# Optimization experiments

Measured on AMD Instinct MI355X. Metric: run time of the kernel, lower is better.

Reference implementation:

```python
import jax, jax.numpy as jnp
import numpy as np

HID = 256
B, H, W, Q = 4, 192, 192, 36864


def conv3x3(x, w, b):
    # x [B,C,H,W], w [O,C,3,3]
    y = jax.lax.conv_general_dilated(x, w, (1, 1), ((1, 1), (1, 1)),
                                     dimension_numbers=('NCHW', 'OIHW', 'NCHW'))
    return y + b[None, :, None, None]


def gather_nchw(x, iy, ix):
    # nearest-neighbor gather: x [B,C,H,W], iy/ix [B,Q] -> [B,Q,C]
    b, c, h, w = x.shape
    lin = iy * w + ix
    g = jnp.take_along_axis(x.reshape(b, c, h * w), lin[:, None, :], axis=2)
    return jnp.transpose(g, (0, 2, 1))


def bilinear_border(x, cy, cx):
    # grid_sample bilinear, padding_mode='border', align_corners=False
    b, c, h, w = x.shape
    fy = ((cy + 1.0) * h - 1.0) * 0.5
    fx = ((cx + 1.0) * w - 1.0) * 0.5
    y0 = jnp.floor(fy)
    x0 = jnp.floor(fx)
    wy = fy - y0
    wx = fx - x0
    y0i = jnp.clip(y0, 0, h - 1).astype(jnp.int32)
    y1i = jnp.clip(y0 + 1, 0, h - 1).astype(jnp.int32)
    x0i = jnp.clip(x0, 0, w - 1).astype(jnp.int32)
    x1i = jnp.clip(x0 + 1, 0, w - 1).astype(jnp.int32)
    v00 = gather_nchw(x, y0i, x0i)
    v01 = gather_nchw(x, y0i, x1i)
    v10 = gather_nchw(x, y1i, x0i)
    v11 = gather_nchw(x, y1i, x1i)
    wy = wy[..., None]
    wx = wx[..., None]
    return (v00 * (1 - wy) * (1 - wx) + v01 * (1 - wy) * wx
            + v10 * wy * (1 - wx) + v11 * wy * wx)


def setup_inputs():
    key = jax.random.key(0)
    ks = jax.random.split(key, 20)
    sc = 0.05
    d = {}
    d['inp'] = jax.random.normal(ks[0], (B, 3, H, W), jnp.float32)
    d['score'] = jax.random.normal(ks[1], (B, 3, H, W), jnp.float32)
    d['coord'] = jax.random.uniform(ks[2], (B, Q, 2), jnp.float32, -1.0, 1.0)
    d['cell'] = jnp.full((B, Q, 2), 2.0 / H, jnp.float32)
    d['coef_w'] = jax.random.normal(ks[3], (HID, 9, 3, 3), jnp.float32) * sc
    d['coef_b'] = jnp.zeros((HID,), jnp.float32)
    d['freq_w'] = jax.random.normal(ks[4], (HID, 9, 3, 3), jnp.float32) * sc
    d['freq_b'] = jnp.zeros((HID,), jnp.float32)
    d['phase_w'] = jax.random.normal(ks[5], (HID // 2, 2), jnp.float32) * sc  # Linear(2, HID//2, bias=False)
    d['a1_w'] = jax.random.normal(ks[6], (128, 3, 3, 3), jnp.float32) * sc
    d['a1_b'] = jnp.zeros((128,), jnp.float32)
    d['a2_w'] = jax.random.normal(ks[7], (3, 128, 3, 3), jnp.float32) * sc
    d['a2_b'] = jnp.zeros((3,), jnp.float32)
    dims = [HID, 256, 256, 256, 256, 3]
    for i in range(5):
        d[f'im_w{i}'] = jax.random.normal(ks[8 + i], (dims[i + 1], dims[i]), jnp.float32) * sc
        d[f'im_b{i}'] = jnp.zeros((dims[i + 1],), jnp.float32)
    return d


def lte_forward(inp, score, coord, cell,
                coef_w, coef_b, freq_w, freq_b, phase_w,
                a1_w, a1_b, a2_w, a2_b,
                im_w0, im_b0, im_w1, im_b1, im_w2, im_b2, im_w3, im_b3, im_w4, im_b4):
    # adapter: conv -> sin -> conv -> sin (Sine w0=1)
    weights = jnp.sin(conv3x3(jnp.sin(conv3x3(inp, a1_w, a1_b)), a2_w, a2_b))
    feat = jnp.concatenate([inp, score, weights], axis=1)  # [B,9,H,W]
    coef = conv3x3(feat, coef_w, coef_b)  # [B,HID,H,W]
    freq = conv3x3(feat, freq_w, freq_b)
    h, w = feat.shape[-2], feat.shape[-1]
    eps = 1e-6
    # single ensemble member (vx=vy=0): clamp coord and nearest-sample
    cy = jnp.clip(coord[..., 0], -1 + eps, 1 - eps)
    cx = jnp.clip(coord[..., 1], -1 + eps, 1 - eps)
    iy = jnp.clip(jnp.round(((cy + 1.0) * h - 1.0) * 0.5), 0, h - 1).astype(jnp.int32)
    ix = jnp.clip(jnp.round(((cx + 1.0) * w - 1.0) * 0.5), 0, w - 1).astype(jnp.int32)
    q_coef = gather_nchw(coef, iy, ix)  # [B,Q,HID]
    q_freq = gather_nchw(freq, iy, ix)  # [B,Q,HID]
    # nearest pixel-center coordinates (make_coord values)
    qy = -1.0 + (2.0 * iy.astype(jnp.float32) + 1.0) / h
    qx = -1.0 + (2.0 * ix.astype(jnp.float32) + 1.0) / w
    rel = jnp.stack([(coord[..., 0] - qy) * h, (coord[..., 1] - qx) * w], axis=-1)  # [B,Q,2]
    rel_cell = cell * jnp.asarray([h, w], jnp.float32)
    # split into (even,odd) frequency pairs: [B,Q,HID/2,2], contract with rel_coord
    qf = q_freq.reshape(q_freq.shape[0], q_freq.shape[1], HID // 2, 2)
    qf = jnp.einsum('bqjk,bqk->bqj', qf, rel)  # [B,Q,HID/2]
    qf = qf + jnp.einsum('bqk,jk->bqj', rel_cell, phase_w)  # phase linear, no bias
    qf = jnp.concatenate([jnp.cos(jnp.pi * qf), jnp.sin(jnp.pi * qf)], axis=-1)  # [B,Q,HID]
    x = q_coef * qf
    for lw, lb in ((im_w0, im_b0), (im_w1, im_b1), (im_w2, im_b2), (im_w3, im_b3)):
        x = jax.nn.relu(jnp.einsum('bqi,oi->bqo', x, lw) + lb)
    pred = jnp.einsum('bqi,oi->bqo', x, im_w4) + im_b4  # [B,Q,3]
    area = jnp.abs(rel[..., 0] * rel[..., 1]) + 1e-9
    ret = pred * (area / area)[..., None]  # single member -> weight 1 (kept for fidelity)
    ret = ret + bilinear_border(inp, coord[..., 0], coord[..., 1])
    return ret


def reference(inp, score, coord, cell,
              coef_w, coef_b, freq_w, freq_b, phase_w,
              a1_w, a1_b, a2_w, a2_b,
              im_w0, im_b0, im_w1, im_b1, im_w2, im_b2, im_w3, im_b3, im_w4, im_b4):
    return lte_forward(inp, score, coord, cell,
                       coef_w, coef_b, freq_w, freq_b, phase_w,
                       a1_w, a1_b, a2_w, a2_b,
                       im_w0, im_b0, im_w1, im_b1, im_w2, im_b2, im_w3, im_b3, im_w4, im_b4)
```

## Files before the change

kernel.cpp:

```cpp
#include <hip/hip_runtime.h>

typedef unsigned short u16;
typedef unsigned int   u32;
typedef __attribute__((ext_vector_type(8))) short v8s;
typedef __attribute__((ext_vector_type(8))) unsigned short v8u;
typedef __attribute__((ext_vector_type(4))) float v4f;

#define PI_F 3.14159265358979323846f

__device__ __forceinline__ float bf2f(u16 v){ u32 u = ((u32)v) << 16; return __builtin_bit_cast(float, u); }
__device__ __forceinline__ u16 f2bf(float f){
    u32 u = __builtin_bit_cast(u32, f);
    u32 r = (u + 0x7fffu + ((u >> 16) & 1u)) >> 16;
    return (u16)r;
}
__device__ __forceinline__ bool is_f32(const void* cellp){
    u32 u = *(const u32*)cellp;
    return ((u >> 16) != (u & 0xffffu));
}
__device__ __forceinline__ float ldin(const void* p, int i, bool f32){
    return f32 ? ((const float*)p)[i] : bf2f(((const u16*)p)[i]);
}

#define FEAT16_OFF 0
#define W2P_OFF   4718592
#define A1W_OFF   4816896
#define A1B_OFF   4830720
#define A2W_OFF   4831232
#define A2B_OFF   4845056
#define PWF_OFF   4845312
#define IBF_OFF   4846336
#define IWC_OFF   4850688
#define CBP_OFF   5376512
#define W4P_OFF   5378560

__global__ __launch_bounds__(256) void k_pack(
    const void* cw, const void* fw, const void* a1w, const void* a1b,
    const void* a2w, const void* a2b, const void* cb, const void* fb, const void* pwp,
    const void* iw0, const void* ib0, const void* iw1, const void* ib1,
    const void* iw2, const void* ib2, const void* iw3, const void* ib3,
    const void* iw4, const void* ib4, const void* cellp, char* ws){
    bool f32 = is_f32(cellp);
    u16*   w2p  = (u16*)(ws + W2P_OFF);
    float* a1wf = (float*)(ws + A1W_OFF);
    float* a1bf = (float*)(ws + A1B_OFF);
    float* a2wf = (float*)(ws + A2W_OFF);
    float* a2bf = (float*)(ws + A2B_OFF);
    float* pwf  = (float*)(ws + PWF_OFF);
    float* ibf  = (float*)(ws + IBF_OFF);
    u16*   iwc  = (u16*)(ws + IWC_OFF);
    float* cbp  = (float*)(ws + CBP_OFF);
    u16*   w4p  = (u16*)(ws + W4P_OFF);

    int t = blockIdx.x*256 + threadIdx.x;
    if (t < 49152){
        int c = t >> 9, rem = t & 511;
        int tile = c/3, ks = c%3;
        int lm = rem >> 5, r2 = rem & 31, quad = r2 >> 3, jj = r2 & 7;
        int n = tile*16 + lm;
        int r = quad*8 + jj;
        u16 v = 0;
        if (r < 27){
            int pix = r/9, ch = r%9;
            int tap = ks*3 + pix;
            int src = ch*9 + tap;
            if (n < 256) v = f2bf(ldin(cw, n*81 + src, f32));
            else { int u_ = n - 256; int tt = u_ >> 4, nn = u_ & 15;
                   int f = 2*((tt>>1)*16 + nn) + (tt & 1);
                   v = f2bf(ldin(fw, f*81 + src, f32)); }
        }
        w2p[t] = v; return;
    }
    t -= 49152;
    if (t < 3456){ a1wf[t] = ldin(a1w, t, f32); return; }
    t -= 3456;
    if (t < 128){ a1bf[t] = ldin(a1b, t, f32); return; }
    t -= 128;
    if (t < 3456){
        int o = t/1152, r = t%1152, c = r/9, tap = r%9;
        a2wf[(o*9 + tap)*128 + c] = ldin(a2w, t, f32); return;
    }
    t -= 3456;
    if (t < 3){ a2bf[t] = ldin(a2b, t, f32); return; }
    t -= 3;
    if (t < 256){ pwf[t] = ldin(pwp, t, f32); return; }
    t -= 256;
    if (t < 1027){
        const void* src = (t < 256) ? ib0 : (t < 512) ? ib1 : (t < 768) ? ib2 : (t < 1024) ? ib3 : ib4;
        int idx = (t < 1024) ? (t & 255) : (t - 1024);
        ibf[t] = ldin(src, idx, f32); return;
    }
    t -= 1027;
    if (t < 262144){
        int c = t >> 9, rem = t & 511;
        int lm = rem >> 5, r2 = rem & 31, quad = r2 >> 3, jj = r2 & 7;
        int nt = c & 3, ks = (c >> 2) & 7, wv = (c >> 5) & 3, l = c >> 7;
        int col = wv*64 + nt*16 + lm;
        int k = ks*32 + quad*8 + jj;
        const void* src = (l==0) ? iw0 : (l==1) ? iw1 : (l==2) ? iw2 : iw3;
        iwc[t] = f2bf(ldin(src, col*256 + k, f32)); return;
    }
    t -= 262144;
    if (t < 768){  return; }
    t -= 768;
    if (t < 512){
        float v;
        if (t < 256) v = ldin(cb, t, f32);
        else { int u_ = t - 256; int tt = u_ >> 4, nn = u_ & 15;
               int f = 2*((tt>>1)*16 + nn) + (tt & 1); v = ldin(fb, f, f32); }
        cbp[t] = v; return;
    }
    t -= 512;
    if (t < 4096){
        int ks = t >> 9, rem = t & 511;
        int lm = rem >> 5, r2 = rem & 31, quad = r2 >> 3, jj = r2 & 7;
        int k = ks*32 + quad*8 + jj;
        w4p[t] = (lm < 3) ? f2bf(ldin(iw4, lm*256 + k, f32)) : (u16)0;
        return;
    }
}

__global__ __launch_bounds__(256) void k_adapter(const void* __restrict__ inp, const void* __restrict__ score,
                                                 const void* __restrict__ cellp, char* __restrict__ ws){
    __shared__ u16 hlds[324*72];
    bool f32 = is_f32(cellp);
    const float* a1wf = (const float*)(ws + A1W_OFF);
    const float* a1bf = (const float*)(ws + A1B_OFF);
    const float* a2wf = (const float*)(ws + A2W_OFF);
    const float* a2bf = (const float*)(ws + A2B_OFF);
    u16* feat16 = (u16*)(ws + FEAT16_OFF);

    int blk = blockIdx.x; int b = blk/144; int rem = blk%144;
    int ty0 = (rem/12)*16, tx0 = (rem%12)*16;
    int tid = threadIdx.x;
    int ly = tid >> 4, lx = tid & 15;
    float o0 = a2bf[0], o1 = a2bf[1], o2 = a2bf[2];

    #pragma unroll 1
    for (int half = 0; half < 2; ++half){
        int c0base = half*64;
        if (half) __syncthreads();
        #pragma unroll 1
        for (int p = tid; p < 324; p += 256){
            int hy = p/18, hx = p%18;
            int gy = ty0 - 1 + hy, gx = tx0 - 1 + hx;
            bool in_img = (gy >= 0) & (gy < 192) & (gx >= 0) & (gx < 192);
            u16* row = hlds + p*72;
            if (!in_img){
                v8u z = {0,0,0,0,0,0,0,0};
                #pragma unroll
                for (int cc = 0; cc < 64; cc += 8) *(v8u*)(row + cc) = z;
            } else {
                float in27[27];
                #pragma unroll
                for (int ci = 0; ci < 3; ++ci)
                    #pragma unroll
                    for (int tp = 0; tp < 9; ++tp){
                        int yy = gy + tp/3 - 1, xx = gx + tp%3 - 1;
                        bool ok = (yy >= 0) & (yy < 192) & (xx >= 0) & (xx < 192);
                        in27[ci*9+tp] = ok ? ldin(inp, (b*3+ci)*36864 + yy*192 + xx, f32) : 0.f;
                    }
                #pragma unroll 1
                for (int cg = 0; cg < 64; cg += 8){
                    int c = c0base + cg;
                    float s[8];
                    #pragma unroll
                    for (int j = 0; j < 8; ++j) s[j] = a1bf[c+j];
                    #pragma unroll
                    for (int k = 0; k < 27; ++k){
                        float iv = in27[k];
                        #pragma unroll
                        for (int j = 0; j < 8; ++j) s[j] += iv * a1wf[(c+j)*27 + k];
                    }
                    v8u pk;
                    #pragma unroll
                    for (int j = 0; j < 8; ++j) pk[j] = f2bf(__sinf(s[j]));
                    *(v8u*)(row + cg) = pk;
                }
            }
        }
        __syncthreads();
        #pragma unroll 1
        for (int tap = 0; tap < 9; ++tap){
            const u16* row = hlds + ((ly + tap/3)*18 + (lx + tap%3))*72;
            const float* wA = a2wf + tap*128 + c0base;
            const float* wB = wA + 1152;
            const float* wC = wA + 2304;
            #pragma unroll
            for (int cc = 0; cc < 64; cc += 8){
                v8u hv = *(const v8u*)(row + cc);
                #pragma unroll
                for (int j = 0; j < 8; ++j){
                    float h = bf2f(hv[j]);
                    o0 += h*wA[cc+j]; o1 += h*wB[cc+j]; o2 += h*wC[cc+j];
                }
            }
        }
    }
    int gy = ty0 + ly, gx = tx0 + lx;
    int pi = b*3*36864 + gy*192 + gx;
    v8u lo, hi;
    lo[0] = f2bf(ldin(inp, pi, f32));
    lo[1] = f2bf(ldin(inp, pi + 36864, f32));
    lo[2] = f2bf(ldin(inp, pi + 2*36864, f32));
    lo[3] = f2bf(ldin(score, pi, f32));
    lo[4] = f2bf(ldin(score, pi + 36864, f32));
    lo[5] = f2bf(ldin(score, pi + 2*36864, f32));
    lo[6] = f2bf(__sinf(o0));
    lo[7] = f2bf(__sinf(o1));
    hi[0] = f2bf(__sinf(o2));
    hi[1]=hi[2]=hi[3]=hi[4]=hi[5]=hi[6]=hi[7]=0;
    u16* fp = feat16 + ((b*192 + gy)*192 + gx)*16;
    *(v8u*)fp = lo;
    *(v8u*)(fp + 8) = hi;
}

__global__ __launch_bounds__(256, 3) void k_mega(const char* __restrict__ ws,
                                                 const void* __restrict__ inp,
                                                 const void* __restrict__ coord,
                                                 const void* __restrict__ cellp,
                                                 void* __restrict__ out){
    __shared__ __attribute__((aligned(16))) char smem[46080];
    bool f32 = is_f32(cellp);
    const u16*   feat16 = (const u16*)(ws + FEAT16_OFF);
    const u16*   w2p    = (const u16*)(ws + W2P_OFF);
    const float* pwf    = (const float*)(ws + PWF_OFF);
    const float* ibf    = (const float*)(ws + IBF_OFF);
    const u16*   iwc    = (const u16*)(ws + IWC_OFF);
    const float* cbp    = (const float*)(ws + CBP_OFF);
    const u16*   w4p    = (const u16*)(ws + W4P_OFF);

    const int tid = threadIdx.x;
    const int qg0 = blockIdx.x * 64;
    const int b = qg0 / 36864;

    {
        int q = tid >> 2, j = tid & 3;
        int qg = qg0 + q;
        u16* ap = (u16*)(smem + 32768);
        float c0 = ldin(coord, qg*2, f32), c1 = ldin(coord, qg*2+1, f32);
        const float e = 1e-6f;
        float cy = fminf(fmaxf(c0, -1.f+e), 1.f-e);
        float cx = fminf(fmaxf(c1, -1.f+e), 1.f-e);
        int iy = (int)rintf(((cy+1.f)*192.f-1.f)*0.5f); iy = min(max(iy,0),191);
        int ix = (int)rintf(((cx+1.f)*192.f-1.f)*0.5f); ix = min(max(ix,0),191);
        if (j < 3){
            int yy = iy - 1 + j;
            bool yok = (yy >= 0) & (yy <= 191);
            union { u16 a[32]; v8u v[4]; } buf;
            #pragma unroll
            for (int c = 0; c < 32; ++c) buf.a[c] = 0;
            if (yok){
                const u16* base = feat16 + ((b*192 + yy)*192)*16;
                #pragma unroll
                for (int pix = 0; pix < 3; ++pix){
                    int xx = ix - 1 + pix;
                    if (xx >= 0 && xx <= 191){
                        const u16* s = base + xx*16;
                        v8u v = *(const v8u*)s;
                        u16 c8 = s[8];
                        #pragma unroll
                        for (int c = 0; c < 8; ++c) buf.a[pix*9+c] = v[c];
                        buf.a[pix*9+8] = c8;
                    }
                }
            }
            u16* dst = ap + q*96 + j*32;
            *(v8u*)(dst)      = buf.v[0];
            *(v8u*)(dst + 8)  = buf.v[1];
            *(v8u*)(dst + 16) = buf.v[2];
            *(v8u*)(dst + 24) = buf.v[3];
        } else {
            float qy = -1.f + (2.f*iy + 1.f)/192.f;
            float qx = -1.f + (2.f*ix + 1.f)/192.f;
            float4 mm;
            mm.x = (c0 - qy)*192.f; mm.y = (c1 - qx)*192.f;
            mm.z = ldin(cellp, qg*2, f32)*192.f; mm.w = ldin(cellp, qg*2+1, f32)*192.f;
            ((float4*)(smem + 45056))[q] = mm;
        }
    }
    __syncthreads();

    const int wv = tid >> 6, ln = tid & 63;
    const int lm = ln & 15, quad = ln >> 4;
    const int laneoff = lm*32 + quad*8;
    u16* X = (u16*)smem;

    {
        v8s afr[3];
        #pragma unroll
        for (int ks = 0; ks < 3; ++ks)
            afr[ks] = *(const v8s*)(smem + 32768 + ((wv*16 + lm)*96 + ks*32 + quad*8)*2);
        float4 mm[4];
        #pragma unroll
        for (int r = 0; r < 4; ++r)
            mm[r] = ((const float4*)(smem + 45056))[wv*16 + quad*4 + r];
        float p0[8], p1[8];
        #pragma unroll
        for (int g = 0; g < 8; ++g){
            int j = g*16 + lm;
            p0[g] = pwf[2*j]; p1[g] = pwf[2*j+1];
        }
        v8s Bc0[3], Bc1[3], Bf0[3], Bf1[3];
        {
            const u16* p;
            p = w2p + 0*1536  + laneoff; Bc0[0]=*(const v8s*)p; Bc0[1]=*(const v8s*)(p+512); Bc0[2]=*(const v8s*)(p+1024);
            p = w2p + 8*1536  + laneoff; Bc1[0]=*(const v8s*)p; Bc1[1]=*(const v8s*)(p+512); Bc1[2]=*(const v8s*)(p+1024);
            p = w2p + 16*1536 + laneoff; Bf0[0]=*(const v8s*)p; Bf0[1]=*(const v8s*)(p+512); Bf0[2]=*(const v8s*)(p+1024);
            p = w2p + 17*1536 + laneoff; Bf1[0]=*(const v8s*)p; Bf1[1]=*(const v8s*)(p+512); Bf1[2]=*(const v8s*)(p+1024);
        }
        #pragma unroll 1
        for (int g = 0; g < 8; ++g){
            float bb0 = cbp[g*16+lm], bb1 = cbp[(8+g)*16+lm];
            float bb2 = cbp[(16+2*g)*16+lm], bb3 = cbp[(17+2*g)*16+lm];
            v4f a0 = (v4f){bb0,bb0,bb0,bb0};
            v4f a1 = (v4f){bb1,bb1,bb1,bb1};
            v4f a2 = (v4f){bb2,bb2,bb2,bb2};
            v4f a3 = (v4f){bb3,bb3,bb3,bb3};
            #pragma unroll
            for (int ks = 0; ks < 3; ++ks){
                a0 = __builtin_amdgcn_mfma_f32_16x16x32_bf16(afr[ks], Bc0[ks], a0, 0,0,0);
                a1 = __builtin_amdgcn_mfma_f32_16x16x32_bf16(afr[ks], Bc1[ks], a1, 0,0,0);
                a2 = __builtin_amdgcn_mfma_f32_16x16x32_bf16(afr[ks], Bf0[ks], a2, 0,0,0);
                a3 = __builtin_amdgcn_mfma_f32_16x16x32_bf16(afr[ks], Bf1[ks], a3, 0,0,0);
            }
            if (g < 7){
                const u16* p;
                p = w2p + (g+1)*1536    + laneoff; Bc0[0]=*(const v8s*)p; Bc0[1]=*(const v8s*)(p+512); Bc0[2]=*(const v8s*)(p+1024);
                p = w2p + (9+g)*1536    + laneoff; Bc1[0]=*(const v8s*)p; Bc1[1]=*(const v8s*)(p+512); Bc1[2]=*(const v8s*)(p+1024);
                p = w2p + (18+2*g)*1536 + laneoff; Bf0[0]=*(const v8s*)p; Bf0[1]=*(const v8s*)(p+512); Bf0[2]=*(const v8s*)(p+1024);
                p = w2p + (19+2*g)*1536 + laneoff; Bf1[0]=*(const v8s*)p; Bf1[1]=*(const v8s*)(p+512); Bf1[2]=*(const v8s*)(p+1024);
            }
            int j = g*16 + lm;
            int koff_c = (j>>5)*2048 + (j&31);
            int koff_s = ((128+j)>>5)*2048 + (j&31);
            #pragma unroll
            for (int r = 0; r < 4; ++r){
                float qf = a2[r]*mm[r].x + a3[r]*mm[r].y + mm[r].z*p0[g] + mm[r].w*p1[g];
                float sn, cs;
                __sincosf(PI_F * qf, &sn, &cs);
                int q = wv*16 + quad*4 + r;
                X[koff_c + q*32] = f2bf(a0[r] * cs);
                X[koff_s + q*32] = f2bf(a1[r] * sn);
            }
        }
    }
    __syncthreads();

    #pragma unroll 1
    for (int l = 0; l < 4; ++l){
        const u16* Wb = iwc + (l*4 + wv)*16384 + laneoff;
        v4f acc[4][4];
        #pragma unroll
        for (int nt = 0; nt < 4; ++nt){
            float bv = ibf[l*256 + wv*64 + nt*16 + lm];
            #pragma unroll
            for (int mt = 0; mt < 4; ++mt) acc[nt][mt] = (v4f){bv,bv,bv,bv};
        }
        v8s bw[2][4];
        #pragma unroll
        for (int nt = 0; nt < 4; ++nt){
            bw[0][nt] = *(const v8s*)(Wb + (0*4 + nt)*512);
            bw[1][nt] = *(const v8s*)(Wb + (1*4 + nt)*512);
        }
        #pragma unroll
        for (int ks = 0; ks < 8; ++ks){
            v8s a[4];
            #pragma unroll
            for (int mt = 0; mt < 4; ++mt)
                a[mt] = *(const v8s*)(smem + (ks*2048 + (mt*16 + lm)*32 + quad*8)*2);
            v8s nb[4];
            if (ks < 6){
                #pragma unroll
                for (int nt = 0; nt < 4; ++nt)
                    nb[nt] = *(const v8s*)(Wb + ((ks+2)*4 + nt)*512);
            }
            #pragma unroll
            for (int nt = 0; nt < 4; ++nt)
                #pragma unroll
                for (int mt = 0; mt < 4; ++mt)
                    acc[nt][mt] = __builtin_amdgcn_mfma_f32_16x16x32_bf16(a[mt], bw[ks&1][nt], acc[nt][mt], 0,0,0);
            if (ks < 6){
                #pragma unroll
                for (int nt = 0; nt < 4; ++nt) bw[ks&1][nt] = nb[nt];
            }
        }
        __syncthreads();
        #pragma unroll
        for (int nt = 0; nt < 4; ++nt){
            int col = wv*64 + nt*16 + lm;
            u16* base = X + (col>>5)*2048 + (col&31);
            #pragma unroll
            for (int mt = 0; mt < 4; ++mt)
                #pragma unroll
                for (int r = 0; r < 4; ++r){
                    int q = mt*16 + quad*4 + r;
                    base[q*32] = f2bf(fmaxf(acc[nt][mt][r], 0.f));
                }
        }
        __syncthreads();
    }

    {
        float bv = (lm < 3) ? ibf[1024 + lm] : 0.f;
        v4f accf = (v4f){bv,bv,bv,bv};
        v8s bA = *(const v8s*)(w4p + laneoff);
        #pragma unroll
        for (int ks = 0; ks < 8; ++ks){
            v8s a = *(const v8s*)(smem + (ks*2048 + (wv*16 + lm)*32 + quad*8)*2);
            v8s bN;
            if (ks < 7) bN = *(const v8s*)(w4p + (ks+1)*512 + laneoff);
            accf = __builtin_amdgcn_mfma_f32_16x16x32_bf16(a, bA, accf, 0,0,0);
            bA = bN;
        }
        if (lm < 3){
            #pragma unroll
            for (int r = 0; r < 4; ++r){
                int q = wv*16 + quad*4 + r;
                int qg = qg0 + q;
                float c0 = ldin(coord, qg*2, f32), c1 = ldin(coord, qg*2+1, f32);
                float fy = ((c0 + 1.f)*192.f - 1.f)*0.5f;
                float fx = ((c1 + 1.f)*192.f - 1.f)*0.5f;
                float y0 = floorf(fy), x0 = floorf(fx);
                float wy = fy - y0, wx = fx - x0;
                int y0i = (int)fminf(fmaxf(y0, 0.f), 191.f);
                int y1i = (int)fminf(fmaxf(y0 + 1.f, 0.f), 191.f);
                int x0i = (int)fminf(fmaxf(x0, 0.f), 191.f);
                int x1i = (int)fminf(fmaxf(x0 + 1.f, 0.f), 191.f);
                int ibase = (b*3 + lm)*36864;
                float v00 = ldin(inp, ibase + y0i*192 + x0i, f32);
                float v01 = ldin(inp, ibase + y0i*192 + x1i, f32);
                float v10 = ldin(inp, ibase + y1i*192 + x0i, f32);
                float v11 = ldin(inp, ibase + y1i*192 + x1i, f32);
                float bil = v00*(1.f-wy)*(1.f-wx) + v01*(1.f-wy)*wx + v10*wy*(1.f-wx) + v11*wy*wx;
                float val = accf[r] + bil;
                if (f32) ((float*)out)[qg*3 + lm] = val;
                else     ((u16*)out)[qg*3 + lm] = f2bf(val);
            }
        }
    }
}

extern "C" void kernel_launch(void* const* d_in, const int* in_sizes, int n_in,
                              void* d_out, int out_size, void* d_ws, size_t ws_size,
                              hipStream_t stream){
    (void)in_sizes; (void)n_in; (void)out_size; (void)ws_size;
    const void* inp   = d_in[0];
    const void* score = d_in[1];
    const void* coord = d_in[2];
    const void* cellp = d_in[3];
    const void* cw    = d_in[4];
    const void* cb    = d_in[5];
    const void* fw    = d_in[6];
    const void* fb    = d_in[7];
    const void* pw    = d_in[8];
    const void* a1w   = d_in[9];
    const void* a1b   = d_in[10];
    const void* a2w   = d_in[11];
    const void* a2b   = d_in[12];
    const void* iw0   = d_in[13];
    const void* ib0   = d_in[14];
    const void* iw1   = d_in[15];
    const void* ib1   = d_in[16];
    const void* iw2   = d_in[17];
    const void* ib2   = d_in[18];
    const void* iw3   = d_in[19];
    const void* ib3   = d_in[20];
    const void* iw4   = d_in[21];
    const void* ib4   = d_in[22];
    char* ws = (char*)d_ws;

    hipLaunchKernelGGL(k_pack, dim3(1270), dim3(256), 0, stream,
                       cw, fw, a1w, a1b, a2w, a2b, cb, fb, pw,
                       iw0, ib0, iw1, ib1, iw2, ib2, iw3, ib3, iw4, ib4,
                       cellp, ws);
    hipLaunchKernelGGL(k_adapter, dim3(576), dim3(256), 0, stream, inp, score, cellp, ws);
    hipLaunchKernelGGL(k_mega, dim3(2304), dim3(256), 0, stream, (const char*)ws, inp, coord, cellp, d_out);
}
```

Before: 372.4 us.

## Move adapter convolutions onto bf16 MFMA with im2col staging in shared memory

The adapter kernel's two 3x3 convolutions (3->128 with sine, 128->3) were done with scalar FP32 FMAs per thread. They are now computed with bf16 MFMA 16x16x32 instructions. Inputs are staged into shared memory as an im2col-like A matrix, and k_pack prepacks swizzled weight matrices for both convs. Tiles shrink to 8x16 pixels, so the grid doubles and more blocks fit per CU. The cost is bf16 rounding of the conv inputs and weights, plus padding waste in the MFMA tiles: K is padded to 64 for the first conv and N to 16 for the three output channels.

```diff
diff --git a/kernel.cpp b/kernel.cpp
--- a/kernel.cpp
+++ b/kernel.cpp
@@ -2,6 +2,7 @@
 
 typedef unsigned short u16;
 typedef unsigned int   u32;
+typedef unsigned long long u64;
 typedef __attribute__((ext_vector_type(8))) short v8s;
 typedef __attribute__((ext_vector_type(8))) unsigned short v8u;
 typedef __attribute__((ext_vector_type(4))) float v4f;
@@ -33,6 +34,8 @@
 #define IWC_OFF   4850688
 #define CBP_OFF   5376512
 #define W4P_OFF   5378560
+#define W1SW_OFF  5386752
+#define W2SW_OFF  5403136
 
 __global__ __launch_bounds__(256) void k_pack(
     const void* cw, const void* fw, const void* a1w, const void* a1b,
@@ -51,6 +54,8 @@
     u16*   iwc  = (u16*)(ws + IWC_OFF);
     float* cbp  = (float*)(ws + CBP_OFF);
     u16*   w4p  = (u16*)(ws + W4P_OFF);
+    u16*   w1sw = (u16*)(ws + W1SW_OFF);
+    u16*   w2sw = (u16*)(ws + W2SW_OFF);
 
     int t = blockIdx.x*256 + threadIdx.x;
     if (t < 49152){
@@ -101,7 +106,7 @@
         iwc[t] = f2bf(ldin(src, col*256 + k, f32)); return;
     }
     t -= 262144;
-    if (t < 768){  return; }
+    if (t < 768){ return; }
     t -= 768;
     if (t < 512){
         float v;
@@ -118,101 +123,163 @@
         w4p[t] = (lm < 3) ? f2bf(ldin(iw4, lm*256 + k, f32)) : (u16)0;
         return;
     }
-}
-
-__global__ __launch_bounds__(256) void k_adapter(const void* __restrict__ inp, const void* __restrict__ score,
-                                                 const void* __restrict__ cellp, char* __restrict__ ws){
-    __shared__ u16 hlds[324*72];
+    t -= 4096;
+    if (t < 8192){
+        int c = t >> 9, rem = t & 511;
+        int lm = rem >> 5, r2 = rem & 31, quad = r2 >> 3, jj = r2 & 7;
+        int h = c >> 3, nt = (c & 7) >> 1, ks = c & 1;
+        int ch = h*64 + nt*16 + lm;
+        int kk = quad*8 + jj;
+        u16 v = 0;
+        int jr = -1, r = 0;
+        if (ks == 0){ jr = kk >> 4; r = kk & 15; }
+        else if (kk < 16){ jr = 2; r = kk; }
+        if (jr >= 0 && r < 12){
+            int px = r >> 2, ci = r & 3;
+            if (ci < 3) v = f2bf(ldin(a1w, ch*27 + ci*9 + jr*3 + px, f32));
+        }
+        w1sw[t] = v; return;
+    }
+    t -= 8192;
+    if (t < 18432){
+        int c = t >> 9, rem = t & 511;
+        int lm = rem >> 5, r2 = rem & 31, quad = r2 >> 3, jj = r2 & 7;
+        int h = c / 18, tap = (c % 18) >> 1, ks = c & 1;
+        int k = ks*32 + quad*8 + jj;
+        int ch = h*64 + k;
+        u16 v = 0;
+        if (lm < 3) v = f2bf(ldin(a2w, lm*1152 + ch*9 + tap, f32));
+        w2sw[t] = v; return;
+    }
+}
+
+__global__ __launch_bounds__(256, 3) void k_adapter(const void* __restrict__ inp, const void* __restrict__ score,
+                                                    const void* __restrict__ cellp, char* __restrict__ ws){
+    __shared__ __attribute__((aligned(16))) char smem[46480];
     bool f32 = is_f32(cellp);
-    const float* a1wf = (const float*)(ws + A1W_OFF);
     const float* a1bf = (const float*)(ws + A1B_OFF);
-    const float* a2wf = (const float*)(ws + A2W_OFF);
     const float* a2bf = (const float*)(ws + A2B_OFF);
+    const u16*   w1sw = (const u16*)(ws + W1SW_OFF);
+    const u16*   w2sw = (const u16*)(ws + W2SW_OFF);
     u16* feat16 = (u16*)(ws + FEAT16_OFF);
 
-    int blk = blockIdx.x; int b = blk/144; int rem = blk%144;
-    int ty0 = (rem/12)*16, tx0 = (rem%12)*16;
+    int blk = blockIdx.x; int b = blk/288; int rem = blk%288;
+    int ty0 = (rem/12)*8, tx0 = (rem%12)*16;
     int tid = threadIdx.x;
-    int ly = tid >> 4, lx = tid & 15;
-    float o0 = a2bf[0], o1 = a2bf[1], o2 = a2bf[2];
-
+    u16* S   = (u16*)smem;
+    u16* A   = (u16*)(smem + 1920);
+    u16* hid = (u16*)(smem + 22000);
+
+    if (tid < 240) ((u64*)smem)[tid] = 0ULL;
+    __syncthreads();
     #pragma unroll 1
-    for (int half = 0; half < 2; ++half){
-        int c0base = half*64;
-        if (half) __syncthreads();
+    for (int e = tid; e < 720; e += 256){
+        int ci = e/240, r2 = e%240, hy = r2/20, hx = r2%20;
+        int gy = ty0 - 2 + hy, gx = tx0 - 2 + hx;
+        if (gy >= 0 && gy < 192 && gx >= 0 && gx < 192)
+            S[(hy*20+hx)*4 + ci] = f2bf(ldin(inp, (b*3+ci)*36864 + gy*192 + gx, f32));
+    }
+    __syncthreads();
+    #pragma unroll 1
+    for (int p = tid; p < 193; p += 256){
+        u64* drow = (u64*)(A + p*52);
+        if (p < 180){
+            int hy = p/18, hx = p%18;
+            #pragma unroll
+            for (int jr = 0; jr < 3; ++jr){
+                const u64* srow = (const u64*)(S + ((hy+jr)*20 + hx)*4);
+                u64 v0 = srow[0], v1 = srow[1], v2 = srow[2];
+                drow[jr*4+0] = v0; drow[jr*4+1] = v1; drow[jr*4+2] = v2; drow[jr*4+3] = 0ULL;
+            }
+            drow[12] = 0ULL;
+        } else {
+            #pragma unroll
+            for (int k = 0; k < 13; ++k) drow[k] = 0ULL;
+        }
+    }
+    __syncthreads();
+
+    const int wv = tid >> 6, ln = tid & 63;
+    const int lm = ln & 15, quad = ln >> 4;
+    const int laneoff = lm*32 + quad*8;
+
+    float bias2 = (lm < 3) ? a2bf[lm] : 0.f;
+    v4f acc2[2];
+    acc2[0] = (v4f){bias2,bias2,bias2,bias2};
+    acc2[1] = acc2[0];
+
+    #pragma unroll 1
+    for (int h = 0; h < 2; ++h){
+        float bias1 = a1bf[h*64 + wv*16 + lm];
+        v8s B0 = *(const v8s*)(w1sw + (h*8 + wv*2 + 0)*512 + laneoff);
+        v8s B1 = *(const v8s*)(w1sw + (h*8 + wv*2 + 1)*512 + laneoff);
         #pragma unroll 1
-        for (int p = tid; p < 324; p += 256){
-            int hy = p/18, hx = p%18;
-            int gy = ty0 - 1 + hy, gx = tx0 - 1 + hx;
-            bool in_img = (gy >= 0) & (gy < 192) & (gx >= 0) & (gx < 192);
-            u16* row = hlds + p*72;
-            if (!in_img){
-                v8u z = {0,0,0,0,0,0,0,0};
-                #pragma unroll
-                for (int cc = 0; cc < 64; cc += 8) *(v8u*)(row + cc) = z;
-            } else {
-                float in27[27];
-                #pragma unroll
-                for (int ci = 0; ci < 3; ++ci)
-                    #pragma unroll
-                    for (int tp = 0; tp < 9; ++tp){
-                        int yy = gy + tp/3 - 1, xx = gx + tp%3 - 1;
-                        bool ok = (yy >= 0) & (yy < 192) & (xx >= 0) & (xx < 192);
-                        in27[ci*9+tp] = ok ? ldin(inp, (b*3+ci)*36864 + yy*192 + xx, f32) : 0.f;
-                    }
-                #pragma unroll 1
-                for (int cg = 0; cg < 64; cg += 8){
-                    int c = c0base + cg;
-                    float s[8];
-                    #pragma unroll
-                    for (int j = 0; j < 8; ++j) s[j] = a1bf[c+j];
-                    #pragma unroll
-                    for (int k = 0; k < 27; ++k){
-                        float iv = in27[k];
-                        #pragma unroll
-                        for (int j = 0; j < 8; ++j) s[j] += iv * a1wf[(c+j)*27 + k];
-                    }
-                    v8u pk;
-                    #pragma unroll
-                    for (int j = 0; j < 8; ++j) pk[j] = f2bf(__sinf(s[j]));
-                    *(v8u*)(row + cg) = pk;
+        for (int mt = 0; mt < 12; ++mt){
+            const u16* ar = A + (mt*16 + lm)*52 + quad*8;
+            v8s a0 = *(const v8s*)(ar);
+            v8s a1 = *(const v8s*)(ar + 32);
+            v4f c = (v4f){bias1,bias1,bias1,bias1};
+            c = __builtin_amdgcn_mfma_f32_16x16x32_bf16(a0, B0, c, 0,0,0);
+            c = __builtin_amdgcn_mfma_f32_16x16x32_bf16(a1, B1, c, 0,0,0);
+            #pragma unroll
+            for (int r = 0; r < 4; ++r){
+                int px = mt*16 + quad*4 + r;
+                if (px < 180){
+                    int hy = px/18, hx = px - hy*18;
+                    int gy = ty0 - 1 + hy, gx = tx0 - 1 + hx;
+                    bool ok = (gy >= 0) & (gy < 192) & (gx >= 0) & (gx < 192);
+                    hid[px*68 + wv*16 + lm] = ok ? f2bf(__sinf(c[r])) : (u16)0;
                 }
             }
         }
         __syncthreads();
         #pragma unroll 1
         for (int tap = 0; tap < 9; ++tap){
-            const u16* row = hlds + ((ly + tap/3)*18 + (lx + tap%3))*72;
-            const float* wA = a2wf + tap*128 + c0base;
-            const float* wB = wA + 1152;
-            const float* wC = wA + 2304;
-            #pragma unroll
-            for (int cc = 0; cc < 64; cc += 8){
-                v8u hv = *(const v8u*)(row + cc);
-                #pragma unroll
-                for (int j = 0; j < 8; ++j){
-                    float h = bf2f(hv[j]);
-                    o0 += h*wA[cc+j]; o1 += h*wB[cc+j]; o2 += h*wC[cc+j];
-                }
-            }
-        }
-    }
-    int gy = ty0 + ly, gx = tx0 + lx;
-    int pi = b*3*36864 + gy*192 + gx;
-    v8u lo, hi;
-    lo[0] = f2bf(ldin(inp, pi, f32));
-    lo[1] = f2bf(ldin(inp, pi + 36864, f32));
-    lo[2] = f2bf(ldin(inp, pi + 2*36864, f32));
-    lo[3] = f2bf(ldin(score, pi, f32));
-    lo[4] = f2bf(ldin(score, pi + 36864, f32));
-    lo[5] = f2bf(ldin(score, pi + 2*36864, f32));
-    lo[6] = f2bf(__sinf(o0));
-    lo[7] = f2bf(__sinf(o1));
-    hi[0] = f2bf(__sinf(o2));
-    hi[1]=hi[2]=hi[3]=hi[4]=hi[5]=hi[6]=hi[7]=0;
-    u16* fp = feat16 + ((b*192 + gy)*192 + gx)*16;
-    *(v8u*)fp = lo;
-    *(v8u*)(fp + 8) = hi;
+            int ty = tap/3, tx = tap%3;
+            v8s Bt0 = *(const v8s*)(w2sw + ((h*9 + tap)*2 + 0)*512 + laneoff);
+            v8s Bt1 = *(const v8s*)(w2sw + ((h*9 + tap)*2 + 1)*512 + laneoff);
+            #pragma unroll
+            for (int i = 0; i < 2; ++i){
+                int py = wv*2 + i;
+                const u16* hrow = hid + ((py+ty)*18 + lm + tx)*68;
+                v8s a0 = *(const v8s*)(hrow + quad*8);
+                v8s a1 = *(const v8s*)(hrow + 32 + quad*8);
+                acc2[i] = __builtin_amdgcn_mfma_f32_16x16x32_bf16(a0, Bt0, acc2[i], 0,0,0);
+                acc2[i] = __builtin_amdgcn_mfma_f32_16x16x32_bf16(a1, Bt1, acc2[i], 0,0,0);
+            }
+        }
+        __syncthreads();
+    }
+    u16* out3 = S;
+    if (lm < 3){
+        #pragma unroll
+        for (int i = 0; i < 2; ++i)
+            #pragma unroll
+            for (int r = 0; r < 4; ++r){
+                int m = (wv*2 + i)*16 + quad*4 + r;
+                out3[m*4 + lm] = f2bf(__sinf(acc2[i][r]));
+            }
+    }
+    __syncthreads();
+    if (tid < 128){
+        int py = tid >> 4, px = tid & 15;
+        int gy = ty0 + py, gx = tx0 + px;
+        int pi = b*3*36864 + gy*192 + gx;
+        v8u lo, hi;
+        lo[0] = f2bf(ldin(inp, pi, f32));
+        lo[1] = f2bf(ldin(inp, pi + 36864, f32));
+        lo[2] = f2bf(ldin(inp, pi + 2*36864, f32));
+        lo[3] = f2bf(ldin(score, pi, f32));
+        lo[4] = f2bf(ldin(score, pi + 36864, f32));
+        lo[5] = f2bf(ldin(score, pi + 2*36864, f32));
+        lo[6] = out3[tid*4 + 0];
+        lo[7] = out3[tid*4 + 1];
+        hi[0] = out3[tid*4 + 2];
+        hi[1]=hi[2]=hi[3]=hi[4]=hi[5]=hi[6]=hi[7]=0;
+        u16* fp = feat16 + ((b*192 + gy)*192 + gx)*16;
+        *(v8u*)fp = lo;
+        *(v8u*)(fp + 8) = hi;
+    }
 }
 
 __global__ __launch_bounds__(256, 3) void k_mega(const char* __restrict__ ws,
@@ -470,10 +537,10 @@
     const void* ib4   = d_in[22];
     char* ws = (char*)d_ws;
 
-    hipLaunchKernelGGL(k_pack, dim3(1270), dim3(256), 0, stream,
+    hipLaunchKernelGGL(k_pack, dim3(1374), dim3(256), 0, stream,
                        cw, fw, a1w, a1b, a2w, a2b, cb, fb, pw,
                        iw0, ib0, iw1, ib1, iw2, ib2, iw3, ib3, iw4, ib4,
                        cellp, ws);
-    hipLaunchKernelGGL(k_adapter, dim3(576), dim3(256), 0, stream, inp, score, cellp, ws);
+    hipLaunchKernelGGL(k_adapter, dim3(1152), dim3(256), 0, stream, inp, score, cellp, ws);
     hipLaunchKernelGGL(k_mega, dim3(2304), dim3(256), 0, stream, (const char*)ws, inp, coord, cellp, d_out);
 }
```

New measurement: 323.9 us. 1.15x faster.
